# Kernel optimization log

Hardware: AMD Instinct MI355X
Metric: run time of the kernel (lower is better)

## Reference

```python
import jax, jax.numpy as jnp
import numpy as np

N = 40000      # nodes
E = 320000     # edges (avg degree 8)
F = 512        # feats_in_size
H = 256        # num_hidden_nodes
HEADS = 8      # num_attention_heads
NEG_SLOPE = 0.01  # torch LeakyReLU default


def setup_inputs() -> dict:
    key = jax.random.key(0)
    k = jax.random.split(key, 8)
    feats = jax.random.normal(k[0], (N, F), jnp.float32)
    # strictly upper-triangular edges (dst > src) so the original module's
    # in-place sequential update equals the parallel segment-softmax GAT
    src = jax.random.randint(k[1], (E,), 0, N - 1, dtype=jnp.int32)
    dst = src + jax.random.randint(k[2], (E,), 1, N - src, dtype=jnp.int32)
    adj_ind = jnp.stack([src, dst], axis=0)  # [2, E]
    adjacency_matrix = jnp.zeros((1, 1), jnp.float32)  # unused when adj_ind given
    W_w = jax.random.normal(k[3], (F, H), jnp.float32) * 0.05   # Linear weight (transposed)
    W_b = jax.random.normal(k[4], (H,), jnp.float32) * 0.05
    attn_w = jax.random.normal(k[5], (HEADS, 2 * H), jnp.float32) * 0.05  # per-head [1,2H] stacked
    attn_b = jax.random.normal(k[6], (HEADS,), jnp.float32) * 0.05
    return {"feats": feats, "adjacency_matrix": adjacency_matrix, "adj_ind": adj_ind,
            "W_w": W_w, "W_b": W_b, "attn_w": attn_w, "attn_b": attn_b}


def reference(feats, adjacency_matrix, adj_ind, W_w, W_b, attn_w, attn_b):
    src, dst = adj_ind[0], adj_ind[1]
    h = feats @ W_w + W_b                       # [N, H]
    h_src = h[src]                              # [E, H] gather
    h_dst = h[dst]                              # [E, H] gather
    # attn_i(cat(h_src, h_dst)) == h_src @ a_i[:H] + h_dst @ a_i[H:] + b_i
    a_s, a_d = attn_w[:, :H], attn_w[:, H:]     # [HEADS, H] each
    scores = h_src @ a_s.T + h_dst @ a_d.T + attn_b  # [E, HEADS]
    scores = jax.nn.leaky_relu(scores, NEG_SLOPE)
    # segment softmax over outgoing edges of each src node
    m = jax.ops.segment_max(scores, src, num_segments=N)   # [N, HEADS]
    ex = jnp.exp(scores - m[src])
    denom = jax.ops.segment_sum(ex, src, num_segments=N)   # [N, HEADS]
    alpha = ex / denom[src]                                 # [E, HEADS]
    # per-head: out_i[u] = h[u] + sum_{(u,v)} alpha_i(u,v) * h[v]
    outs = [h + jax.ops.segment_sum(alpha[:, i:i + 1] * h_dst, src, num_segments=N)
            for i in range(HEADS)]
    return jnp.concatenate(outs, axis=1)        # [N, HEADS*H]
```

## Files before the change

### kernel.cpp

```cpp
#include <hip/hip_runtime.h>

typedef __attribute__((ext_vector_type(8))) short short8v;
typedef __attribute__((ext_vector_type(4))) float f32x4;

#define NN 40000
#define FF 512
#define HH 256
#define EE 320000
#define NHEADS 8
#define NEG_SLOPE 0.01f
#define NB 157

__device__ __forceinline__ short f2bf(float x) {
    unsigned u = __float_as_uint(x);
    u += 0x7fffu + ((u >> 16) & 1u);
    return (short)(u >> 16);
}
__device__ __forceinline__ float bf2f(unsigned short b) {
    return __uint_as_float(((unsigned)b) << 16);
}

__global__ void prep_kernel(const float* __restrict__ W, short* __restrict__ Wt,
                            int* __restrict__ p) {
    int b = blockIdx.x;
    if (b < 512) {
        int i = b * 256 + threadIdx.x;
        int k = i >> 8, n = i & 255;
        Wt[n * 512 + k] = f2bf(W[i]);
    } else {
        int i = (b - 512) * 256 + threadIdx.x;
        if (i < 2 * NN) p[i] = 0;
    }
}

__global__ __launch_bounds__(512) void gemm_kernel(
    const float* __restrict__ feats,
    const short* __restrict__ Btf,
    const float* __restrict__ bias,
    float* __restrict__ hout)
{
    __shared__ short8v ldsA[512];
    __shared__ short8v ldsB[2048];
    const int tid = threadIdx.x;
    const int lane = tid & 63, w = tid >> 6;
    const int wm = w >> 2, wn = w & 3;
    const int r0 = blockIdx.x * 64;

    const int arow = tid >> 3, aslot = tid & 7;

    float4 regA[2];
    short8v regB[4];

    auto stage_loadA = [&](int k0) {
        const float* p = feats + (size_t)(r0 + arow) * 512 + k0 + aslot * 8;
        regA[0] = *reinterpret_cast<const float4*>(p);
        regA[1] = *reinterpret_cast<const float4*>(p + 4);
    };
    auto stage_loadB = [&](int k0) {
        #pragma unroll
        for (int c = 0; c < 4; ++c) {
            int u = tid + c * 512;
            int row = u >> 3, slot = u & 7;
            regB[c] = *reinterpret_cast<const short8v*>(Btf + (size_t)row * 512 + k0 + slot * 8);
        }
    };
    auto stage_store = [&]() {
        short8v v;
        #pragma unroll
        for (int j = 0; j < 4; ++j) {
            v[j]     = f2bf(regA[0][j]);
            v[4 + j] = f2bf(regA[1][j]);
        }
        ldsA[arow * 8 + (aslot ^ (arow & 7))] = v;
        #pragma unroll
        for (int c = 0; c < 4; ++c) {
            int u = tid + c * 512;
            int row = u >> 3, slot = u & 7;
            ldsB[row * 8 + (slot ^ (row & 7))] = regB[c];
        }
    };

    f32x4 acc[2][4];
    #pragma unroll
    for (int i = 0; i < 2; ++i)
        #pragma unroll
        for (int j = 0; j < 4; ++j)
            acc[i][j] = {0.f, 0.f, 0.f, 0.f};

    stage_loadA(0);
    stage_loadB(0);

    for (int kt = 0; kt < 8; ++kt) {
        __syncthreads();
        stage_store();
        __syncthreads();
        if (kt < 7) {
            stage_loadA((kt + 1) * 64);
            stage_loadB((kt + 1) * 64);
        }
        #pragma unroll
        for (int kc = 0; kc < 2; ++kc) {
            short8v af[2], bfr[4];
            int kslot = kc * 4 + (lane >> 4);
            #pragma unroll
            for (int mr = 0; mr < 2; ++mr) {
                int row = wm * 32 + mr * 16 + (lane & 15);
                af[mr] = ldsA[row * 8 + (kslot ^ (row & 7))];
            }
            #pragma unroll
            for (int nr = 0; nr < 4; ++nr) {
                int col = wn * 64 + nr * 16 + (lane & 15);
                bfr[nr] = ldsB[col * 8 + (kslot ^ (col & 7))];
            }
            #pragma unroll
            for (int mr = 0; mr < 2; ++mr)
                #pragma unroll
                for (int nr = 0; nr < 4; ++nr)
                    acc[mr][nr] = __builtin_amdgcn_mfma_f32_16x16x32_bf16(
                        af[mr], bfr[nr], acc[mr][nr], 0, 0, 0);
        }
    }

    #pragma unroll
    for (int mr = 0; mr < 2; ++mr) {
        #pragma unroll
        for (int nr = 0; nr < 4; ++nr) {
            int gc = wn * 64 + nr * 16 + (lane & 15);
            float b = bias[gc];
            #pragma unroll
            for (int j = 0; j < 4; ++j) {
                int gr = r0 + wm * 32 + mr * 16 + (lane >> 4) * 4 + j;
                hout[(size_t)gr * 256 + gc] = acc[mr][nr][j] + b;
            }
        }
    }
}

__global__ __launch_bounds__(256) void sproj_kernel(
    const float* __restrict__ h, const float* __restrict__ attn_w,
    float* __restrict__ s_src, float* __restrict__ s_dst,
    unsigned short* __restrict__ h2)
{
    int wid = threadIdx.x >> 6, lane = threadIdx.x & 63;
    int n = blockIdx.x * 4 + wid;
    if (n >= NN) return;
    float4 hv = *reinterpret_cast<const float4*>(h + (size_t)n * 256 + lane * 4);

    ushort4 hb;
    hb.x = (unsigned short)f2bf(hv.x);
    hb.y = (unsigned short)f2bf(hv.y);
    hb.z = (unsigned short)f2bf(hv.z);
    hb.w = (unsigned short)f2bf(hv.w);
    *reinterpret_cast<ushort4*>(h2 + (size_t)n * 256 + lane * 4) = hb;

    float ss[8], sd[8];
    #pragma unroll
    for (int q = 0; q < 8; ++q) {
        float4 as = *reinterpret_cast<const float4*>(attn_w + q * 512 + lane * 4);
        float4 ad = *reinterpret_cast<const float4*>(attn_w + q * 512 + 256 + lane * 4);
        ss[q] = hv.x * as.x + hv.y * as.y + hv.z * as.z + hv.w * as.w;
        sd[q] = hv.x * ad.x + hv.y * ad.y + hv.z * ad.z + hv.w * ad.w;
    }
    #pragma unroll
    for (int q = 0; q < 8; ++q) {
        #pragma unroll
        for (int off = 32; off >= 1; off >>= 1) {
            ss[q] += __shfl_xor(ss[q], off);
            sd[q] += __shfl_xor(sd[q], off);
        }
    }
    if (lane == 0) {
        #pragma unroll
        for (int q = 0; q < 8; ++q) {
            s_src[(size_t)n * 8 + q] = ss[q];
            s_dst[(size_t)n * 8 + q] = sd[q];
        }
    }
}

__global__ void edge_kernel(const int* __restrict__ src, const int* __restrict__ dst,
                            const float* __restrict__ s_src, const float* __restrict__ s_dst,
                            const float* __restrict__ attn_b,
                            float* __restrict__ escores, int* __restrict__ deg)
{
    int e = blockIdx.x * 256 + threadIdx.x;
    if (e >= EE) return;
    int s = src[e], d = dst[e];
    float4 a0 = reinterpret_cast<const float4*>(s_src + (size_t)s * 8)[0];
    float4 a1 = reinterpret_cast<const float4*>(s_src + (size_t)s * 8)[1];
    float4 c0 = reinterpret_cast<const float4*>(s_dst + (size_t)d * 8)[0];
    float4 c1 = reinterpret_cast<const float4*>(s_dst + (size_t)d * 8)[1];
    float4 b0 = reinterpret_cast<const float4*>(attn_b)[0];
    float4 b1 = reinterpret_cast<const float4*>(attn_b)[1];
    float v[8];
    v[0] = a0.x + c0.x + b0.x; v[1] = a0.y + c0.y + b0.y;
    v[2] = a0.z + c0.z + b0.z; v[3] = a0.w + c0.w + b0.w;
    v[4] = a1.x + c1.x + b1.x; v[5] = a1.y + c1.y + b1.y;
    v[6] = a1.z + c1.z + b1.z; v[7] = a1.w + c1.w + b1.w;
    #pragma unroll
    for (int q = 0; q < 8; ++q) {
        float sc = v[q] > 0.f ? v[q] : NEG_SLOPE * v[q];
        v[q] = __expf(sc);
    }
    float4 o0 = {v[0], v[1], v[2], v[3]};
    float4 o1 = {v[4], v[5], v[6], v[7]};
    reinterpret_cast<float4*>(escores + (size_t)e * 8)[0] = o0;
    reinterpret_cast<float4*>(escores + (size_t)e * 8)[1] = o1;
    atomicAdd(&deg[s], 1);
}

__global__ __launch_bounds__(256) void scan1_kernel(const int* __restrict__ deg,
                                                    int* __restrict__ rowtmp,
                                                    int* __restrict__ partials)
{
    __shared__ int buf[256];
    int tid = threadIdx.x;
    int i = blockIdx.x * 256 + tid;
    int v = (i < NN) ? deg[i] : 0;
    buf[tid] = v;
    __syncthreads();
    #pragma unroll
    for (int off = 1; off < 256; off <<= 1) {
        int t = (tid >= off) ? buf[tid - off] : 0;
        __syncthreads();
        buf[tid] += t;
        __syncthreads();
    }
    if (i < NN) rowtmp[i] = buf[tid] - v;
    if (tid == 255) partials[blockIdx.x] = buf[255];
}

__global__ __launch_bounds__(256) void scan23_kernel(const int* __restrict__ rowtmp,
                                                     const int* __restrict__ partials,
                                                     int* __restrict__ rowstart)
{
    __shared__ int buf[256];
    __shared__ int offs[256];
    int tid = threadIdx.x;
    int v = (tid < NB) ? partials[tid] : 0;
    buf[tid] = v;
    __syncthreads();
    #pragma unroll
    for (int off = 1; off < 256; off <<= 1) {
        int t = (tid >= off) ? buf[tid - off] : 0;
        __syncthreads();
        buf[tid] += t;
        __syncthreads();
    }
    offs[tid] = buf[tid] - v;
    __syncthreads();
    int myoff = offs[blockIdx.x];
    int i = blockIdx.x * 256 + tid;
    if (i < NN) rowstart[i] = rowtmp[i] + myoff;
    if (blockIdx.x == 0 && tid == 0) rowstart[NN] = EE;
}

__global__ void fill_kernel(const int* __restrict__ src, const int* __restrict__ rowstart,
                            int* __restrict__ cursor, int* __restrict__ csr)
{
    int e = blockIdx.x * 256 + threadIdx.x;
    if (e >= EE) return;
    int s = src[e];
    int pos = atomicAdd(&cursor[s], 1);
    csr[rowstart[s] + pos] = e;
}

__global__ __launch_bounds__(256) void agg_kernel(
    const float* __restrict__ h, const unsigned short* __restrict__ h2,
    const float* __restrict__ escores,
    const int* __restrict__ csr, const int* __restrict__ rowstart,
    const int* __restrict__ dstArr, float* __restrict__ out)
{
    int wid = threadIdx.x >> 6, lane = threadIdx.x & 63;
    int n = blockIdx.x * 4 + wid;
    if (n >= NN) return;
    int start = rowstart[n];
    int deg = rowstart[n + 1] - start;
    int ei = lane >> 3, hh = lane & 7;

    float4 hv = *reinterpret_cast<const float4*>(h + (size_t)n * 256 + lane * 4);
    float4 acc[8];
    #pragma unroll
    for (int q = 0; q < 8; ++q) acc[q] = {0.f, 0.f, 0.f, 0.f};
    float den = 0.f;

    for (int base = 0; base < deg; base += 8) {
        int idx = base + ei;
        int e = 0; float ex = 0.f;
        if (idx < deg) { e = csr[start + idx]; ex = escores[(size_t)e * 8 + hh]; }
        den += ex;
        int cnt = min(8, deg - base);
        for (int t = 0; t < cnt; ++t) {
            int ee = __shfl(e, t * 8);
            int dd = dstArr[ee];
            ushort4 hb = *reinterpret_cast<const ushort4*>(h2 + (size_t)dd * 256 + lane * 4);
            float4 hd = {bf2f(hb.x), bf2f(hb.y), bf2f(hb.z), bf2f(hb.w)};
            #pragma unroll
            for (int q = 0; q < 8; ++q) {
                float exq = __shfl(ex, t * 8 + q);
                acc[q].x += exq * hd.x; acc[q].y += exq * hd.y;
                acc[q].z += exq * hd.z; acc[q].w += exq * hd.w;
            }
        }
    }

    den += __shfl_xor(den, 8);
    den += __shfl_xor(den, 16);
    den += __shfl_xor(den, 32);

    float* orow = out + (size_t)n * 2048;
    #pragma unroll
    for (int q = 0; q < 8; ++q) {
        float dq = __shfl(den, q);
        float r = dq > 0.f ? 1.f / dq : 0.f;
        float4 o;
        o.x = hv.x + acc[q].x * r; o.y = hv.y + acc[q].y * r;
        o.z = hv.z + acc[q].z * r; o.w = hv.w + acc[q].w * r;
        *reinterpret_cast<float4*>(orow + q * 256 + lane * 4) = o;
    }
}

extern "C" void kernel_launch(void* const* d_in, const int* in_sizes, int n_in,
                              void* d_out, int out_size, void* d_ws, size_t ws_size,
                              hipStream_t stream) {
    const float* feats  = (const float*)d_in[0];
    const int*   adj    = (const int*)d_in[2];
    const float* W_w    = (const float*)d_in[3];
    const float* W_b    = (const float*)d_in[4];
    const float* attn_w = (const float*)d_in[5];
    const float* attn_b = (const float*)d_in[6];
    float* out = (float*)d_out;
    const int* srcA = adj;
    const int* dstA = adj + EE;

    char* ws = (char*)d_ws;
    size_t off = 0;
    auto alloc = [&](size_t bytes) -> void* {
        void* p = ws + off;
        off += (bytes + 255) & ~(size_t)255;
        return p;
    };
    short* Wt            = (short*)alloc((size_t)HH * FF * 2);
    float* h             = (float*)alloc((size_t)NN * HH * 4);
    unsigned short* h2   = (unsigned short*)alloc((size_t)NN * HH * 2);
    float* s_src   = (float*)alloc((size_t)NN * 8 * 4);
    float* s_dst   = (float*)alloc((size_t)NN * 8 * 4);
    float* escores = (float*)alloc((size_t)EE * 8 * 4);
    int*   deg     = (int*)alloc((size_t)NN * 4 * 2);
    int*   cursor  = deg + NN;
    int*   rowtmp  = (int*)alloc((size_t)NN * 4);
    int*   partials= (int*)alloc((size_t)256 * 4);
    int*   rowstart= (int*)alloc((size_t)(NN + 1) * 4);
    int*   csr     = (int*)alloc((size_t)EE * 4);

    prep_kernel<<<512 + (2 * NN + 255) / 256, 256, 0, stream>>>(W_w, Wt, deg);
    gemm_kernel<<<NN / 64, 512, 0, stream>>>(feats, Wt, W_b, h);
    sproj_kernel<<<NN / 4, 256, 0, stream>>>(h, attn_w, s_src, s_dst, h2);
    edge_kernel<<<(EE + 255) / 256, 256, 0, stream>>>(srcA, dstA, s_src, s_dst, attn_b, escores, deg);
    scan1_kernel<<<NB, 256, 0, stream>>>(deg, rowtmp, partials);
    scan23_kernel<<<NB, 256, 0, stream>>>(rowtmp, partials, rowstart);
    fill_kernel<<<(EE + 255) / 256, 256, 0, stream>>>(srcA, rowstart, cursor, csr);
    agg_kernel<<<NN / 4, 256, 0, stream>>>(h, h2, escores, csr, rowstart, dstA, out);
}
```

Baseline: 224.9 us.

## Store h only as bf16 from GEMM and pack dst into CSR entries

```diff
diff --git a/kernel.cpp b/kernel.cpp
--- a/kernel.cpp
+++ b/kernel.cpp
@@ -37,7 +37,7 @@
     const float* __restrict__ feats,
     const short* __restrict__ Btf,
     const float* __restrict__ bias,
-    float* __restrict__ hout)
+    unsigned short* __restrict__ h2)
 {
     __shared__ short8v ldsA[512];
     __shared__ short8v ldsB[2048];
@@ -130,28 +130,21 @@
             #pragma unroll
             for (int j = 0; j < 4; ++j) {
                 int gr = r0 + wm * 32 + mr * 16 + (lane >> 4) * 4 + j;
-                hout[(size_t)gr * 256 + gc] = acc[mr][nr][j] + b;
+                h2[(size_t)gr * 256 + gc] = (unsigned short)f2bf(acc[mr][nr][j] + b);
             }
         }
     }
 }
 
 __global__ __launch_bounds__(256) void sproj_kernel(
-    const float* __restrict__ h, const float* __restrict__ attn_w,
-    float* __restrict__ s_src, float* __restrict__ s_dst,
-    unsigned short* __restrict__ h2)
+    const unsigned short* __restrict__ h2, const float* __restrict__ attn_w,
+    float* __restrict__ s_src, float* __restrict__ s_dst)
 {
     int wid = threadIdx.x >> 6, lane = threadIdx.x & 63;
     int n = blockIdx.x * 4 + wid;
     if (n >= NN) return;
-    float4 hv = *reinterpret_cast<const float4*>(h + (size_t)n * 256 + lane * 4);
-
-    ushort4 hb;
-    hb.x = (unsigned short)f2bf(hv.x);
-    hb.y = (unsigned short)f2bf(hv.y);
-    hb.z = (unsigned short)f2bf(hv.z);
-    hb.w = (unsigned short)f2bf(hv.w);
-    *reinterpret_cast<ushort4*>(h2 + (size_t)n * 256 + lane * 4) = hb;
+    ushort4 hb = *reinterpret_cast<const ushort4*>(h2 + (size_t)n * 256 + lane * 4);
+    float4 hv = {bf2f(hb.x), bf2f(hb.y), bf2f(hb.z), bf2f(hb.w)};
 
     float ss[8], sd[8];
     #pragma unroll
@@ -255,21 +248,22 @@
     if (blockIdx.x == 0 && tid == 0) rowstart[NN] = EE;
 }
 
-__global__ void fill_kernel(const int* __restrict__ src, const int* __restrict__ rowstart,
-                            int* __restrict__ cursor, int* __restrict__ csr)
+__global__ void fill_kernel(const int* __restrict__ src, const int* __restrict__ dst,
+                            const int* __restrict__ rowstart,
+                            int* __restrict__ cursor, int2* __restrict__ csrPack)
 {
     int e = blockIdx.x * 256 + threadIdx.x;
     if (e >= EE) return;
     int s = src[e];
     int pos = atomicAdd(&cursor[s], 1);
-    csr[rowstart[s] + pos] = e;
+    csrPack[rowstart[s] + pos] = make_int2(e, dst[e]);
 }
 
 __global__ __launch_bounds__(256) void agg_kernel(
-    const float* __restrict__ h, const unsigned short* __restrict__ h2,
+    const unsigned short* __restrict__ h2,
     const float* __restrict__ escores,
-    const int* __restrict__ csr, const int* __restrict__ rowstart,
-    const int* __restrict__ dstArr, float* __restrict__ out)
+    const int2* __restrict__ csrPack, const int* __restrict__ rowstart,
+    float* __restrict__ out)
 {
     int wid = threadIdx.x >> 6, lane = threadIdx.x & 63;
     int n = blockIdx.x * 4 + wid;
@@ -278,28 +272,31 @@
     int deg = rowstart[n + 1] - start;
     int ei = lane >> 3, hh = lane & 7;
 
-    float4 hv = *reinterpret_cast<const float4*>(h + (size_t)n * 256 + lane * 4);
-    float4 acc[8];
+    ushort4 sb = *reinterpret_cast<const ushort4*>(h2 + (size_t)n * 256 + lane * 4);
+    f32x4 hv = {bf2f(sb.x), bf2f(sb.y), bf2f(sb.z), bf2f(sb.w)};
+    f32x4 acc[8];
     #pragma unroll
     for (int q = 0; q < 8; ++q) acc[q] = {0.f, 0.f, 0.f, 0.f};
     float den = 0.f;
 
     for (int base = 0; base < deg; base += 8) {
         int idx = base + ei;
-        int e = 0; float ex = 0.f;
-        if (idx < deg) { e = csr[start + idx]; ex = escores[(size_t)e * 8 + hh]; }
+        int dd = 0; float ex = 0.f;
+        if (idx < deg) {
+            int2 p = csrPack[start + idx];
+            dd = p.y;
+            ex = escores[(size_t)p.x * 8 + hh];
+        }
         den += ex;
         int cnt = min(8, deg - base);
         for (int t = 0; t < cnt; ++t) {
-            int ee = __shfl(e, t * 8);
-            int dd = dstArr[ee];
-            ushort4 hb = *reinterpret_cast<const ushort4*>(h2 + (size_t)dd * 256 + lane * 4);
-            float4 hd = {bf2f(hb.x), bf2f(hb.y), bf2f(hb.z), bf2f(hb.w)};
+            int ddt = __shfl(dd, t * 8);
+            ushort4 hb = *reinterpret_cast<const ushort4*>(h2 + (size_t)ddt * 256 + lane * 4);
+            f32x4 hd = {bf2f(hb.x), bf2f(hb.y), bf2f(hb.z), bf2f(hb.w)};
             #pragma unroll
             for (int q = 0; q < 8; ++q) {
                 float exq = __shfl(ex, t * 8 + q);
-                acc[q].x += exq * hd.x; acc[q].y += exq * hd.y;
-                acc[q].z += exq * hd.z; acc[q].w += exq * hd.w;
+                acc[q] += hd * exq;
             }
         }
     }
@@ -313,10 +310,8 @@
     for (int q = 0; q < 8; ++q) {
         float dq = __shfl(den, q);
         float r = dq > 0.f ? 1.f / dq : 0.f;
-        float4 o;
-        o.x = hv.x + acc[q].x * r; o.y = hv.y + acc[q].y * r;
-        o.z = hv.z + acc[q].z * r; o.w = hv.w + acc[q].w * r;
-        *reinterpret_cast<float4*>(orow + q * 256 + lane * 4) = o;
+        f32x4 o = hv + acc[q] * r;
+        *reinterpret_cast<f32x4*>(orow + q * 256 + lane * 4) = o;
     }
 }
 
@@ -341,7 +336,6 @@
         return p;
     };
     short* Wt            = (short*)alloc((size_t)HH * FF * 2);
-    float* h             = (float*)alloc((size_t)NN * HH * 4);
     unsigned short* h2   = (unsigned short*)alloc((size_t)NN * HH * 2);
     float* s_src   = (float*)alloc((size_t)NN * 8 * 4);
     float* s_dst   = (float*)alloc((size_t)NN * 8 * 4);
@@ -351,14 +345,14 @@
     int*   rowtmp  = (int*)alloc((size_t)NN * 4);
     int*   partials= (int*)alloc((size_t)256 * 4);
     int*   rowstart= (int*)alloc((size_t)(NN + 1) * 4);
-    int*   csr     = (int*)alloc((size_t)EE * 4);
+    int2*  csrPack = (int2*)alloc((size_t)EE * 8);
 
     prep_kernel<<<512 + (2 * NN + 255) / 256, 256, 0, stream>>>(W_w, Wt, deg);
-    gemm_kernel<<<NN / 64, 512, 0, stream>>>(feats, Wt, W_b, h);
-    sproj_kernel<<<NN / 4, 256, 0, stream>>>(h, attn_w, s_src, s_dst, h2);
+    gemm_kernel<<<NN / 64, 512, 0, stream>>>(feats, Wt, W_b, h2);
+    sproj_kernel<<<NN / 4, 256, 0, stream>>>(h2, attn_w, s_src, s_dst);
     edge_kernel<<<(EE + 255) / 256, 256, 0, stream>>>(srcA, dstA, s_src, s_dst, attn_b, escores, deg);
     scan1_kernel<<<NB, 256, 0, stream>>>(deg, rowtmp, partials);
     scan23_kernel<<<NB, 256, 0, stream>>>(rowtmp, partials, rowstart);
-    fill_kernel<<<(EE + 255) / 256, 256, 0, stream>>>(srcA, rowstart, cursor, csr);
-    agg_kernel<<<NN / 4, 256, 0, stream>>>(h, h2, escores, csr, rowstart, dstA, out);
-}
+    fill_kernel<<<(EE + 255) / 256, 256, 0, stream>>>(srcA, dstA, rowstart, cursor, csrPack);
+    agg_kernel<<<NN / 4, 256, 0, stream>>>(h2, escores, csrPack, rowstart, out);
+}
```

Result: faster. 217.3 us (-3.4%).
